# Kernel optimization log

Measured on AMD Instinct MI355X. Metric: run time of the kernel, lower is better.

## Reference

```python
import jax, jax.numpy as jnp
import numpy as np

EXP_ORDER = 2  # matches init_kwargs exp_order
N_FEAT = 8
Q_DIM = 1
BATCH = 262144
T_EXPANDED = 164  # n + C(n+1,2) + C(n+2,3) for n=8, degrees 1..3
N_OUT = 8


def taylor_expand(x, exp_order):
    """Faithful vectorized version of the nested multiply/concat loop.

    x: [B, n, q]. Builds all monomials of degree 1..exp_order+1 using the same
    recursion as the TF code: at each order, for each j, multiply x_j with the
    previous-order block starting at Id[j], then append. The q-loop in the
    original is replaced by broadcasting over the q axis (identical math).
    """
    n = x.shape[1]
    Id = list(range(n))  # start index of x_j's block in the previous-order terms
    epd = x
    for _ in range(exp_order):
        L = epd.shape[1]  # slice end Id[n-1]+1 always equals current length
        blocks = []
        new_Id = []
        offset = L
        for j in range(n):
            blk = x[:, j:j + 1, :] * epd[:, Id[j]:L, :]  # [B, L-Id[j], q]
            new_Id.append(offset)
            offset += blk.shape[1]
            blocks.append(blk)
        epd = jnp.concatenate([epd] + blocks, axis=1)
        Id = new_Id
    return epd


def setup_inputs() -> dict:
    key = jax.random.key(0)
    k1, k2, k3 = jax.random.split(key, 3)
    x = jax.random.normal(k1, (BATCH, N_FEAT, Q_DIM), dtype=jnp.float32)
    # 'dl' init: uniform(-1/sqrt(fan), 1/sqrt(fan)) with fan = weights_shape[0]
    dl_scale = 1.0 / np.sqrt(N_OUT)
    W = jax.random.uniform(k2, (N_OUT, T_EXPANDED), minval=-dl_scale,
                           maxval=dl_scale, dtype=jnp.float32)
    # 'uniform' bias init: U(-0.2, 0.2), shape [out, 1]
    b = jax.random.uniform(k3, (N_OUT, 1), minval=-0.2, maxval=0.2,
                           dtype=jnp.float32)
    return {"x": x, "W": W, "b": b}


def reference(x, W, b):
    # cp_type == 'none': pass-through of the input
    epd = taylor_expand(x, EXP_ORDER)          # [B, T, q]
    out = jnp.einsum('ot,btq->boq', W, epd) + b[None]  # [B, out, q]
    # act_type == 'relu'
    return jax.nn.relu(out)
```

## Files before the change

### kernel.cpp

```cpp
#include <hip/hip_runtime.h>
#include <hip/hip_bf16.h>
#include <string.h>


static constexpr int TEXP = 164;
static constexpr int NOUT = 8;
static constexpr int NMFMA = 11;
static constexpr int HALF = 88;

using f32x16 = __attribute__((ext_vector_type(16))) float;
using short8 = __attribute__((ext_vector_type(8))) short;

constexpr int rowstart2(int j) { return j * 8 - j * (j - 1) / 2; }
constexpr int start3(int j) {
  int s = 44;
  for (int jp = 0; jp < j; ++jp) s += (8 - jp) * (9 - jp) / 2;
  return s;
}
struct D3 { int j, p; };
constexpr D3 d3idx(int M) {
  int j = 0;
  while (start3(j + 1) <= M) ++j;
  int q = M - start3(j);
  int a = j;
  while (q >= (8 - a)) { q -= (8 - a); ++a; }
  int b = a + q;
  return { j, rowstart2(a) + (b - a) };
}

template <int M>
__device__ __forceinline__ float mono(const float (&xv)[8], const float (&d2)[36]) {
  if constexpr (M < 8) {
    return xv[M];
  } else if constexpr (M < 44) {
    return d2[M - 8];
  } else {
    constexpr D3 t = d3idx(M);
    return xv[t.j] * d2[t.p];
  }
}

__device__ __forceinline__ short bf16bits(float v) {
  __hip_bfloat16 h = __float2bfloat16(v);
  short s;
  memcpy(&s, &h, 2);
  return s;
}

template <int C>
__device__ __forceinline__ void do_slot(const float (&xv)[8], const float (&d2)[36],
                                        bool hi, short8& bv) {
  float v0 = mono<C>(xv, d2);
  float v1;
  if constexpr (HALF + C < TEXP) v1 = mono<HALF + C>(xv, d2);
  else v1 = 0.0f;
  float v = hi ? v1 : v0;
  bv[C & 7] = bf16bits(v);
}

template <int I>
__device__ __forceinline__ void slot8(const float (&xv)[8], const float (&d2)[36],
                                      bool hi, short8& bv) {
  do_slot<8 * I + 0>(xv, d2, hi, bv);
  do_slot<8 * I + 1>(xv, d2, hi, bv);
  do_slot<8 * I + 2>(xv, d2, hi, bv);
  do_slot<8 * I + 3>(xv, d2, hi, bv);
  do_slot<8 * I + 4>(xv, d2, hi, bv);
  do_slot<8 * I + 5>(xv, d2, hi, bv);
  do_slot<8 * I + 6>(xv, d2, hi, bv);
  do_slot<8 * I + 7>(xv, d2, hi, bv);
}

template <int I>
struct MfmaStep {
  static __device__ __forceinline__ void run(const float (&xv)[8], const float (&d2)[36],
                                             bool hi, const unsigned short* __restrict__ wpl,
                                             short8 af_cur, f32x16& acc) {
    short8 af_next;
    if constexpr (I + 1 < NMFMA)
      af_next = *reinterpret_cast<const short8*>(wpl + (I + 1) * 64 * 8);
    short8 bv;
    slot8<I>(xv, d2, hi, bv);
    acc = __builtin_amdgcn_mfma_f32_32x32x16_bf16(af_cur, bv, acc, 0, 0, 0);
    __builtin_amdgcn_sched_barrier(0);
    if constexpr (I + 1 < NMFMA)
      MfmaStep<I + 1>::run(xv, d2, hi, wpl, af_next, acc);
  }
};

__global__ void prep_w(const float* __restrict__ W, unsigned short* __restrict__ wp) {
  for (int idx = threadIdx.x + blockIdx.x * blockDim.x; idx < NMFMA * 64 * 8;
       idx += blockDim.x * gridDim.x) {
    int j = idx & 7;
    int lane = (idx >> 3) & 63;
    int i = idx >> 9;
    int row = lane & 31, h = lane >> 5;
    int m = HALF * h + 8 * i + j;
    float v = (row < NOUT && m < TEXP) ? W[row * TEXP + m] : 0.0f;
    union { float f; unsigned int u; } c; c.f = v;
    unsigned int u = c.u;
    wp[idx] = (unsigned short)((u + 0x7fffu + ((u >> 16) & 1u)) >> 16);
  }
}

__global__ __launch_bounds__(256, 4) void taylor_mfma(
    const float* __restrict__ x, const float* __restrict__ b,
    const unsigned short* __restrict__ wp, float* __restrict__ out, int ngroups) {
  const int lane = (int)(threadIdx.x & 63);
  const bool hi = lane >= 32;
  const int h = hi ? 1 : 0;
  const int col = lane & 31;

  const unsigned short* wpl = wp + lane * 8;
  short8 af0 = *reinterpret_cast<const short8*>(wpl);

  const float4 bv4 = *reinterpret_cast<const float4*>(b + 4 * h);

  const int g = (int)((blockIdx.x * blockDim.x + threadIdx.x) >> 6);
  if (g >= ngroups) return;

  const int elem = g * 32 + col;
  float4 xa = reinterpret_cast<const float4*>(x)[elem * 2 + 0];
  float4 xb = reinterpret_cast<const float4*>(x)[elem * 2 + 1];
  float xv[8] = {xa.x, xa.y, xa.z, xa.w, xb.x, xb.y, xb.z, xb.w};

  float d2[36];
#pragma unroll
  for (int j = 0; j < 8; ++j) {
#pragma unroll
    for (int k = j; k < 8; ++k) {
      d2[rowstart2(j) + (k - j)] = xv[j] * xv[k];
    }
  }

  f32x16 acc;
#pragma unroll
  for (int r = 0; r < 16; ++r) acc[r] = 0.0f;

  MfmaStep<0>::run(xv, d2, hi, wpl, af0, acc);

  float4 o;
  o.x = fmaxf(acc[0] + bv4.x, 0.0f);
  o.y = fmaxf(acc[1] + bv4.y, 0.0f);
  o.z = fmaxf(acc[2] + bv4.z, 0.0f);
  o.w = fmaxf(acc[3] + bv4.w, 0.0f);
  *reinterpret_cast<float4*>(out + elem * 8 + 4 * h) = o;
}

extern "C" void kernel_launch(void* const* d_in, const int* in_sizes, int n_in,
                              void* d_out, int out_size, void* d_ws, size_t ws_size,
                              hipStream_t stream) {
  const float* x = (const float*)d_in[0];
  const float* W = (const float*)d_in[1];
  const float* b = (const float*)d_in[2];
  float* out = (float*)d_out;
  unsigned short* wp = (unsigned short*)d_ws;

  int n = in_sizes[0] / 8;
  int ngroups = n / 32;
  int blocks = ngroups / 4;

  prep_w<<<8, 256, 0, stream>>>(W, wp);
  taylor_mfma<<<blocks, 256, 0, stream>>>(x, b, wp, out, ngroups);
}
```

Baseline: 17.26 us.

## Use xor-4 symmetric slot mapping so both half-waves compute monomials without selects

Rebuilds the K-split across the two half-waves. Each half-wave now evaluates the same compile-time slot table on an input vector whose feature halves are swapped (xor 4), and a constexpr table maps each slot to the matching original monomial index when the weights are packed. This removes the per-slot select between two monomials and halves the degree-2 products computed per lane (only rows j<4). It relies on the table covering every monomial exactly once across the halves. It also adds a device-constant lookup in prep_w and launches prep_w with enough threads that the grid-stride loop is no longer needed.

```diff
diff --git a/kernel.cpp b/kernel.cpp
--- a/kernel.cpp
+++ b/kernel.cpp
@@ -6,7 +6,7 @@
 static constexpr int TEXP = 164;
 static constexpr int NOUT = 8;
 static constexpr int NMFMA = 11;
-static constexpr int HALF = 88;
+static constexpr int NSLOT = 88;
 
 using f32x16 = __attribute__((ext_vector_type(16))) float;
 using short8 = __attribute__((ext_vector_type(8))) short;
@@ -17,28 +17,68 @@
   for (int jp = 0; jp < j; ++jp) s += (8 - jp) * (9 - jp) / 2;
   return s;
 }
-struct D3 { int j, p; };
-constexpr D3 d3idx(int M) {
-  int j = 0;
-  while (start3(j + 1) <= M) ++j;
-  int q = M - start3(j);
-  int a = j;
-  while (q >= (8 - a)) { q -= (8 - a); ++a; }
-  int b = a + q;
-  return { j, rowstart2(a) + (b - a) };
-}
-
-template <int M>
-__device__ __forceinline__ float mono(const float (&xv)[8], const float (&d2)[36]) {
-  if constexpr (M < 8) {
-    return xv[M];
-  } else if constexpr (M < 44) {
-    return d2[M - 8];
-  } else {
-    constexpr D3 t = d3idx(M);
-    return xv[t.j] * d2[t.p];
-  }
-}
+constexpr int t3_of(int a, int b, int c) {
+  int x = a, y = b, z = c, t = 0;
+  if (x > y) { t = x; x = y; y = t; }
+  if (y > z) { t = y; y = z; z = t; }
+  if (x > y) { t = x; x = y; y = t; }
+  int off = 0;
+  for (int ap = x; ap < y; ++ap) off += 8 - ap;
+  return start3(x) + off + (z - y);
+}
+
+struct Slot { int deg, a, b, c; };
+struct SlotTable { Slot s[NSLOT]; };
+
+constexpr bool isrep2(int j, int k) {
+  if (k < 4) return true;
+  if (j >= 4) return false;
+  if (k == j + 4) return true;
+  return j < k - 4;
+}
+constexpr bool isrep3(int a, int b, int c) {
+  return ((a < 4) + (b < 4) + (c < 4)) >= 2;
+}
+
+constexpr SlotTable make_slots() {
+  SlotTable T{};
+  int s = 0;
+  for (int j = 0; j < 4; ++j) T.s[s++] = {1, j, 0, 0};
+  for (int j = 0; j < 8; ++j)
+    for (int k = j; k < 8; ++k)
+      if (isrep2(j, k)) T.s[s++] = {2, j, k, 0};
+  for (int a = 0; a < 8; ++a)
+    for (int b = a; b < 8; ++b)
+      for (int c = b; c < 8; ++c)
+        if (isrep3(a, b, c)) T.s[s++] = {3, a, b, c};
+  for (; s < NSLOT; ++s) T.s[s] = {0, 0, 0, 0};
+  return T;
+}
+constexpr SlotTable SLOTS = make_slots();
+
+struct TT { short t[2][NSLOT]; };
+constexpr TT make_tt() {
+  TT r{};
+  for (int h = 0; h < 2; ++h)
+    for (int s = 0; s < NSLOT; ++s) {
+      Slot sl = SLOTS.s[s];
+      int m = h ? 4 : 0;
+      if (sl.deg == 0) { r.t[h][s] = -1; }
+      else if (sl.deg == 1) { r.t[h][s] = (short)(sl.a ^ m); }
+      else if (sl.deg == 2) {
+        if (h == 1 && sl.b == (sl.a ^ 4)) { r.t[h][s] = -1; }
+        else {
+          int a = sl.a ^ m, b = sl.b ^ m;
+          int lo = a < b ? a : b, hi2 = a < b ? b : a;
+          r.t[h][s] = (short)(8 + rowstart2(lo) + (hi2 - lo));
+        }
+      } else {
+        r.t[h][s] = (short)t3_of(sl.a ^ m, sl.b ^ m, sl.c ^ m);
+      }
+    }
+  return r;
+}
+__device__ const TT TDX = make_tt();
 
 __device__ __forceinline__ short bf16bits(float v) {
   __hip_bfloat16 h = __float2bfloat16(v);
@@ -47,60 +87,54 @@
   return s;
 }
 
-template <int C>
-__device__ __forceinline__ void do_slot(const float (&xv)[8], const float (&d2)[36],
-                                        bool hi, short8& bv) {
-  float v0 = mono<C>(xv, d2);
-  float v1;
-  if constexpr (HALF + C < TEXP) v1 = mono<HALF + C>(xv, d2);
-  else v1 = 0.0f;
-  float v = hi ? v1 : v0;
-  bv[C & 7] = bf16bits(v);
-}
-
-template <int I>
-__device__ __forceinline__ void slot8(const float (&xv)[8], const float (&d2)[36],
-                                      bool hi, short8& bv) {
-  do_slot<8 * I + 0>(xv, d2, hi, bv);
-  do_slot<8 * I + 1>(xv, d2, hi, bv);
-  do_slot<8 * I + 2>(xv, d2, hi, bv);
-  do_slot<8 * I + 3>(xv, d2, hi, bv);
-  do_slot<8 * I + 4>(xv, d2, hi, bv);
-  do_slot<8 * I + 5>(xv, d2, hi, bv);
-  do_slot<8 * I + 6>(xv, d2, hi, bv);
-  do_slot<8 * I + 7>(xv, d2, hi, bv);
+template <int S>
+__device__ __forceinline__ float slotval(const float (&xs)[8], const float (&d2)[36]) {
+  constexpr int deg = SLOTS.s[S].deg;
+  constexpr int a = SLOTS.s[S].a;
+  constexpr int b = SLOTS.s[S].b;
+  constexpr int c = SLOTS.s[S].c;
+  if constexpr (deg == 1) return xs[a];
+  else if constexpr (deg == 2) return d2[rowstart2(a) + (b - a)];
+  else if constexpr (deg == 3) return xs[a] * d2[rowstart2(b) + (c - b)];
+  else return 0.0f;
 }
 
 template <int I>
 struct MfmaStep {
-  static __device__ __forceinline__ void run(const float (&xv)[8], const float (&d2)[36],
-                                             bool hi, const unsigned short* __restrict__ wpl,
+  static __device__ __forceinline__ void run(const float (&xs)[8], const float (&d2)[36],
+                                             const unsigned short* __restrict__ wpl,
                                              short8 af_cur, f32x16& acc) {
     short8 af_next;
     if constexpr (I + 1 < NMFMA)
       af_next = *reinterpret_cast<const short8*>(wpl + (I + 1) * 64 * 8);
     short8 bv;
-    slot8<I>(xv, d2, hi, bv);
+    bv[0] = bf16bits(slotval<8 * I + 0>(xs, d2));
+    bv[1] = bf16bits(slotval<8 * I + 1>(xs, d2));
+    bv[2] = bf16bits(slotval<8 * I + 2>(xs, d2));
+    bv[3] = bf16bits(slotval<8 * I + 3>(xs, d2));
+    bv[4] = bf16bits(slotval<8 * I + 4>(xs, d2));
+    bv[5] = bf16bits(slotval<8 * I + 5>(xs, d2));
+    bv[6] = bf16bits(slotval<8 * I + 6>(xs, d2));
+    bv[7] = bf16bits(slotval<8 * I + 7>(xs, d2));
     acc = __builtin_amdgcn_mfma_f32_32x32x16_bf16(af_cur, bv, acc, 0, 0, 0);
     __builtin_amdgcn_sched_barrier(0);
     if constexpr (I + 1 < NMFMA)
-      MfmaStep<I + 1>::run(xv, d2, hi, wpl, af_next, acc);
+      MfmaStep<I + 1>::run(xs, d2, wpl, af_next, acc);
   }
 };
 
 __global__ void prep_w(const float* __restrict__ W, unsigned short* __restrict__ wp) {
-  for (int idx = threadIdx.x + blockIdx.x * blockDim.x; idx < NMFMA * 64 * 8;
-       idx += blockDim.x * gridDim.x) {
-    int j = idx & 7;
-    int lane = (idx >> 3) & 63;
-    int i = idx >> 9;
-    int row = lane & 31, h = lane >> 5;
-    int m = HALF * h + 8 * i + j;
-    float v = (row < NOUT && m < TEXP) ? W[row * TEXP + m] : 0.0f;
-    union { float f; unsigned int u; } c; c.f = v;
-    unsigned int u = c.u;
-    wp[idx] = (unsigned short)((u + 0x7fffu + ((u >> 16) & 1u)) >> 16);
-  }
+  int idx = threadIdx.x + blockIdx.x * blockDim.x;
+  if (idx >= NMFMA * 64 * 8) return;
+  int j = idx & 7;
+  int lane = (idx >> 3) & 63;
+  int i = idx >> 9;
+  int row = lane & 31, h = lane >> 5;
+  int t = TDX.t[h][8 * i + j];
+  float v = (row < NOUT && t >= 0) ? W[row * TEXP + t] : 0.0f;
+  union { float f; unsigned int u; } c; c.f = v;
+  unsigned int u = c.u;
+  wp[idx] = (unsigned short)((u + 0x7fffu + ((u >> 16) & 1u)) >> 16);
 }
 
 __global__ __launch_bounds__(256, 4) void taylor_mfma(
@@ -124,12 +158,16 @@
   float4 xb = reinterpret_cast<const float4*>(x)[elem * 2 + 1];
   float xv[8] = {xa.x, xa.y, xa.z, xa.w, xb.x, xb.y, xb.z, xb.w};
 
+  float xs[8];
+#pragma unroll
+  for (int j = 0; j < 8; ++j) xs[j] = hi ? xv[j ^ 4] : xv[j];
+
   float d2[36];
 #pragma unroll
-  for (int j = 0; j < 8; ++j) {
+  for (int j = 0; j < 4; ++j) {
 #pragma unroll
     for (int k = j; k < 8; ++k) {
-      d2[rowstart2(j) + (k - j)] = xv[j] * xv[k];
+      d2[rowstart2(j) + (k - j)] = xs[j] * xs[k];
     }
   }
 
@@ -137,7 +175,7 @@
 #pragma unroll
   for (int r = 0; r < 16; ++r) acc[r] = 0.0f;
 
-  MfmaStep<0>::run(xv, d2, hi, wpl, af0, acc);
+  MfmaStep<0>::run(xs, d2, wpl, af0, acc);
 
   float4 o;
   o.x = fmaxf(acc[0] + bv4.x, 0.0f);
@@ -160,6 +198,6 @@
   int ngroups = n / 32;
   int blocks = ngroups / 4;
 
-  prep_w<<<8, 256, 0, stream>>>(W, wp);
+  prep_w<<<22, 256, 0, stream>>>(W, wp);
   taylor_mfma<<<blocks, 256, 0, stream>>>(x, b, wp, out, ngroups);
 }
```

Measured after the change: 16.26 us. 1.06x faster.
